# Performance work log

Hardware: AMD Instinct MI355X
Metric: run time of the kernel (lower is better)

The kernel has to match this reference:

```python
import jax, jax.numpy as jnp
import numpy as np

B, S, T, L, D, H = 32, 64, 256, 8, 128, 128
SIGNAL_SD = 1.0 - 0.001   # default signal_sds init
NOISE_SD = 0.01           # GP diagonal jitter (noise_sds) for Cholesky stability


def setup_inputs() -> dict:
    key = jax.random.key(0)
    ks = jax.random.split(key, 8)
    X = jax.random.normal(ks[0], (B, T, D), dtype=jnp.float32)
    times = (jnp.arange(T, dtype=jnp.float32) / T) * 10.0  # span [0, 10)
    log_taus = jax.random.normal(ks[1], (L,), dtype=jnp.float32) * 0.1 + jnp.log(0.5)
    log_R_diag = jax.random.normal(ks[2], (D,), dtype=jnp.float32) * 0.1
    W1 = jax.random.normal(ks[3], (L, H), dtype=jnp.float32) / np.sqrt(L)
    b1 = jnp.zeros((H,), dtype=jnp.float32)
    W2 = jax.random.normal(ks[4], (H, D), dtype=jnp.float32) / np.sqrt(H)
    b2 = jnp.zeros((D,), dtype=jnp.float32)
    eps = jax.random.normal(ks[5], (B, S, L, T), dtype=jnp.float32)
    return {"X": X, "times": times, "log_taus": log_taus, "log_R_diag": log_R_diag,
            "W1": W1, "b1": b1, "W2": W2, "b2": b2, "eps": eps}


def reference(X, times, log_taus, log_R_diag, W1, b1, W2, b2, eps):
    taus = jnp.exp(log_taus)            # [L]
    r = jnp.exp(log_R_diag)             # [D] diagonal of R

    # --- GP prior kernel matrices (squared-exponential SDE kernel), one per latent dim ---
    dt = times[:, None] - times[None, :]                       # [T,T]
    K = (SIGNAL_SD ** 2) * jnp.exp(-(dt ** 2)[None] / (2.0 * (taus ** 2)[:, None, None]))
    K = K + (NOISE_SD ** 2) * jnp.eye(T, dtype=K.dtype)        # [L,T,T]
    Lc = jnp.linalg.cholesky(K)                                # [L,T,T]

    # --- reparameterized prior samples: z = Lc @ eps ---
    z = jnp.einsum('lut,bslt->bslu', Lc, eps)                  # [B,S,L,T]
    Z = jnp.transpose(z, (0, 1, 3, 2))                         # [B,S,T,L]

    # --- decoder MLP: latent -> manifold mean in observation space ---
    h = jnp.tanh(jnp.einsum('bstl,lh->bsth', Z, W1) + b1)      # [B,S,T,H]
    mu = jnp.einsum('bsth,hd->bstd', h, W2) + b2               # [B,S,T,D]

    # --- diagonal-R Gaussian log_prob per timestep, closed form ---
    diff = X[:, None, :, :] - mu                               # [B,S,T,D]
    quad = jnp.sum(diff * diff / r, axis=-1)                   # [B,S,T]
    log_norm = 0.5 * (jnp.sum(log_R_diag) + D * jnp.log(2.0 * jnp.pi))
    logp = -0.5 * quad - log_norm                              # [B,S,T]

    # --- sum over time, logsumexp over MC samples ---
    ll = jnp.sum(logp, axis=2)                                 # [B,S]
    nll = -(jax.scipy.special.logsumexp(ll, axis=1) - jnp.log(jnp.float32(S)))
    return nll                                                 # [B]
```

## Files before the change

### kernel.cpp

```cpp
#include <hip/hip_runtime.h>
#include <hip/hip_bf16.h>
#include <math.h>

#define B_ 32
#define S_ 64
#define T_ 256
#define L_ 8
#define D_ 128
#define H_ 128

typedef __attribute__((ext_vector_type(8))) short short8;
typedef __attribute__((ext_vector_type(4))) short short4v;
typedef __attribute__((ext_vector_type(4))) float float4v;
typedef __attribute__((ext_vector_type(4))) int int4v;

__device__ __forceinline__ short f2bf(float x) {
  __hip_bfloat16 h = __float2bfloat16(x);
  return *reinterpret_cast<short*>(&h);
}

__device__ __forceinline__ float rdlane(float x, int sl) {
  return __int_as_float(__builtin_amdgcn_readlane(__float_as_int(x), sl));
}
__device__ __forceinline__ float dpp_shr1(float x, float tailv) {
  int r = __builtin_amdgcn_update_dpp(__float_as_int(tailv), __float_as_int(x),
                                      0x138, 0xF, 0xF, false);
  return __int_as_float(r);
}

__global__ __launch_bounds__(64) void k_chol_prep(
    const float* __restrict__ times, const float* __restrict__ log_taus,
    __hip_bfloat16* __restrict__ Lcbf_,
    const float* __restrict__ W1, const float* __restrict__ W2,
    __hip_bfloat16* __restrict__ W1T, __hip_bfloat16* __restrict__ W2T)
{
  __shared__ short panel[256][68];
  const int bi = blockIdx.x;
  const int j = threadIdx.x;

  if (bi >= 8) {
    const int base = (bi - 8) * 64 + j;
    for (int idx = base; idx < H_ * D_; idx += 4096) {
      const int cc = idx >> 7, h = idx & 127;
      const int n = cc & 15, nt = cc >> 4;
      const int d = n * 8 + nt;
      W2T[(size_t)cc * H_ + h] = __float2bfloat16(W2[(size_t)h * D_ + d]);
    }
    for (int idx = base; idx < L_ * H_; idx += 4096) {
      const int li = idx >> 7, h = idx & 127;
      const int msrc = 32 * (h >> 5) + 2 * (h & 15) + ((h >> 4) & 1);
      W1T[(size_t)h * L_ + li] = __float2bfloat16(W1[(size_t)li * H_ + msrc]);
    }
    return;
  }

  const int l = bi;
  short* Lbf = (short*)Lcbf_ + (size_t)l * T_ * T_;

  const float tau = expf(log_taus[l]);
  const float inv2tau2 = 0.5f / (tau * tau);
  const float sig2 = 0.999f * 0.999f;
  const float t0 = times[0];

  const float c0 = sig2 + 1e-4f;
  const float isc0 = 1.0f / sqrtf(c0);

  float u[4], v[4];
#pragma unroll
  for (int c = 0; c < 4; ++c) {
    const int d = c * 64 + j;
    const float dt = times[d] - t0;
    float cv = sig2 * __expf(-dt * dt * inv2tau2);
    if (d == 0) cv = c0;
    u[c] = cv * isc0;
    v[c] = (d == 0) ? 0.0f : u[c];
  }

#pragma unroll
  for (int p = 0; p < 4; ++p) {
    for (int kk = 0; kk < 64; ++kk) {
      const float uk = rdlane(u[p], kk);
      const float vk = rdlane(v[p], kk);
      const float dd = fmaxf(__builtin_fmaf(uk, uk, -vk * vk), 1e-20f);
      const float rr = __builtin_amdgcn_rsqf(dd);
      const float s = uk * rr;
      const float sr = vk * rr;

      float up[4];
#pragma unroll
      for (int c = 0; c < 4; ++c) {
        if (c >= p) {
          const float uc = u[c], vc = v[c];
          up[c] = s * uc - sr * vc;
          v[c]  = s * vc - sr * uc;
          const float val = (c > p || j >= kk) ? up[c] : 0.0f;
          panel[(c - p) * 64 + j][kk] = f2bf(val);
        }
      }
#pragma unroll
      for (int c = 3; c >= 0; --c) {
        if (c >= p) {
          const float tail = (c > p) ? rdlane(up[c - 1], 63) : 0.0f;
          u[c] = dpp_shr1(up[c], tail);
        }
      }
    }
    __syncthreads();
    const int rpt = 256 - 64 * p;
    const int rsub = j >> 4, cp = (j & 15) * 4;
    for (int i0 = 0; i0 < rpt; i0 += 4) {
      const int pr = i0 + rsub;
      short4v vv = *(const short4v*)&panel[pr][cp];
      *(short4v*)&Lbf[((size_t)(p * 64 + pr) << 8) + p * 64 + cp] = vv;
    }
    __syncthreads();
  }
}

__global__ __launch_bounds__(256) void k_zgemm(
    const float* __restrict__ eps, const __hip_bfloat16* __restrict__ Lcbf_,
    __hip_bfloat16* __restrict__ Zg)
{
  __shared__ __align__(16) short E[32][264];
  const int bi = blockIdx.x;
  const int l = bi & 7, bs0 = (bi >> 3) * 32;
  const int tid = threadIdx.x, w = tid >> 6, lane = tid & 63;
  const int n = lane & 15, q = lane >> 4;
  const short* Lb = (const short*)Lcbf_ + (size_t)l * T_ * T_;

  {
    const int row = tid >> 3, part = tid & 7;
    const float* src = eps + ((size_t)(bs0 + row) * L_ + l) * T_;
#pragma unroll
    for (int g = 0; g < 8; ++g) {
      const int c = (part + g * 8) * 4;
      float4v f = *(const float4v*)(src + c);
      short4v o;
#pragma unroll
      for (int jj = 0; jj < 4; ++jj) o[jj] = f2bf(f[jj]);
      *(short4v*)&E[row][c] = o;
    }
  }
  __syncthreads();

  float4v acc[4][2];
#pragma unroll
  for (int mi = 0; mi < 4; ++mi)
#pragma unroll
    for (int nt = 0; nt < 2; ++nt) acc[mi][nt] = (float4v){0.f, 0.f, 0.f, 0.f};

  const int kmax = ((15 - w + 2) >> 1) << 5;
  for (int k0 = 0; k0 < kmax; k0 += 32) {
    short8 bfrg[2];
#pragma unroll
    for (int nt = 0; nt < 2; ++nt)
      bfrg[nt] = *(const short8*)&E[nt * 16 + n][k0 + q * 8];
#pragma unroll
    for (int mi = 0; mi < 4; ++mi) {
      const int tile = (mi == 0) ? w : (mi == 1) ? (15 - w) : (mi == 2) ? (7 - w) : (8 + w);
      const int kc = ((tile + 2) >> 1) << 5;
      if (k0 < kc) {
        const int u = tile * 16 + n;
        const short8 afr = *(const short8*)&Lb[((size_t)u << 8) + k0 + q * 8];
#pragma unroll
        for (int nt = 0; nt < 2; ++nt)
          acc[mi][nt] = __builtin_amdgcn_mfma_f32_16x16x32_bf16(afr, bfrg[nt], acc[mi][nt], 0, 0, 0);
      }
    }
  }
  __syncthreads();

#pragma unroll
  for (int mi = 0; mi < 4; ++mi) {
    const int tile = (mi == 0) ? w : (mi == 1) ? (15 - w) : (mi == 2) ? (7 - w) : (8 + w);
#pragma unroll
    for (int nt = 0; nt < 2; ++nt) {
      short4v o;
#pragma unroll
      for (int r = 0; r < 4; ++r) o[r] = f2bf(acc[mi][nt][r]);
      *(short4v*)&E[nt * 16 + n][tile * 16 + q * 4] = o;
    }
  }
  __syncthreads();

  {
    const int row = tid >> 3, part = tid & 7;
    short* dst = (short*)Zg + ((size_t)l * (B_ * S_) + bs0 + row) * T_;
#pragma unroll
    for (int g = 0; g < 4; ++g) {
      const int c = (g * 8 + part) * 8;
      *(short8*)&dst[c] = *(const short8*)&E[row][c];
    }
  }
}

__global__ __launch_bounds__(256, 4) void k_decode(
    const float* __restrict__ X, const __hip_bfloat16* __restrict__ Zg,
    const __hip_bfloat16* __restrict__ W1T, const float* __restrict__ b1,
    const __hip_bfloat16* __restrict__ W2T, const float* __restrict__ b2,
    const float* __restrict__ log_R, float* __restrict__ ll)
{
  __shared__ __align__(16) short Zt[256][8];
  __shared__ __align__(16) __hip_bfloat16 hS[32][136];
  __shared__ float redbuf[4];

  const int bid = blockIdx.x;
  const int bs = (bid & 7) * 256 + (bid >> 3);
  const int b = bs >> 6;
  const int tid = threadIdx.x;
  const int w = tid >> 6, lane = tid & 63;
  const int n = lane & 15, q = lane >> 4;
  const unsigned short* Zs = (const unsigned short*)Zg;
  const short* W1s = (const short*)W1T;
  const short* W2s = (const short*)W2T;

  {
    const size_t base = (size_t)bs * T_ + tid;
    const size_t lstr = (size_t)(B_ * S_) * T_;
    unsigned int p0 = (unsigned int)Zs[base]            | ((unsigned int)Zs[base + lstr]     << 16);
    unsigned int p1 = (unsigned int)Zs[base + 2 * lstr] | ((unsigned int)Zs[base + 3 * lstr] << 16);
    unsigned int p2 = (unsigned int)Zs[base + 4 * lstr] | ((unsigned int)Zs[base + 5 * lstr] << 16);
    unsigned int p3 = (unsigned int)Zs[base + 6 * lstr] | ((unsigned int)Zs[base + 7 * lstr] << 16);
    int4v zi = {(int)p0, (int)p1, (int)p2, (int)p3};
    *(int4v*)&Zt[tid][0] = zi;
  }

  float sLR = log_R[lane] + log_R[lane + 64];
#pragma unroll
  for (int off = 32; off >= 1; off >>= 1) sLR += __shfl_xor(sLR, off);

  const float L22 = 2.8853900817779268f;
  const int d0 = n * 8 + 2 * w;
  const int hc = 32 * w + 2 * n;
  float invr2[2], b22[2], pb[2];
#pragma unroll
  for (int jj = 0; jj < 2; ++jj) {
    invr2[jj] = expf(-log_R[d0 + jj]);
    b22[jj] = b2[d0 + jj];
    pb[jj] = b1[hc + jj] * L22;
  }

  const short8 zero8 = {0, 0, 0, 0, 0, 0, 0, 0};
  short8 w1f[2];
  short8 bfr[2][4];
#pragma unroll
  for (int jj = 0; jj < 2; ++jj) {
    const int c = (2 * w + jj) * 16 + n;
    short8 v = zero8;
    if (q == 0) v = *(const short8*)&W1s[(size_t)c * L_];
    w1f[jj] = v;
#pragma unroll
    for (int ks = 0; ks < 4; ++ks)
      bfr[jj][ks] = *(const short8*)&W2s[(size_t)c * H_ + ks * 32 + q * 8];
  }

  float qsum = 0.0f;
  __syncthreads();

#pragma unroll 1
  for (int ph = 0; ph < 8; ++ph) {
    short* hp = (short*)hS + (q * 4) * 136 + hc;
#pragma unroll 1
    for (int mi = 0; mi < 2; ++mi) {
      short8 zf = zero8;
      if (q == 0) zf = *(const short8*)&Zt[ph * 32 + mi * 16 + n][0];
      float4v c0 = __builtin_amdgcn_mfma_f32_16x16x32_bf16(zf, w1f[0], (float4v){0.f,0.f,0.f,0.f}, 0, 0, 0);
      float4v c1 = __builtin_amdgcn_mfma_f32_16x16x32_bf16(zf, w1f[1], (float4v){0.f,0.f,0.f,0.f}, 0, 0, 0);
#pragma unroll
      for (int r = 0; r < 4; ++r) {
        const float a0 = __builtin_fmaf(c0[r], L22, pb[0]);
        const float a1 = __builtin_fmaf(c1[r], L22, pb[1]);
        const float p0 = __builtin_amdgcn_exp2f(a0) + 1.f;
        const float p1 = __builtin_amdgcn_exp2f(a1) + 1.f;
        const float rj = __builtin_amdgcn_rcpf(p0 * p1);
        const float h0 = __builtin_fmaf(-2.f * p1, rj, 1.f);
        const float h1 = __builtin_fmaf(-2.f * p0, rj, 1.f);
        float2 hv2; hv2.x = h0; hv2.y = h1;
        *reinterpret_cast<__hip_bfloat162*>(hp + r * 136) = __float22bfloat162_rn(hv2);
      }
      hp += 16 * 136;
    }
    __syncthreads();
#pragma unroll 1
    for (int mi = 0; mi < 2; ++mi) {
      short8 af[4];
#pragma unroll
      for (int ks = 0; ks < 4; ++ks)
        af[ks] = *(const short8*)&hS[mi * 16 + n][ks * 32 + q * 8];
      float4v acc0 = (float4v){0.f, 0.f, 0.f, 0.f};
      float4v acc1 = (float4v){0.f, 0.f, 0.f, 0.f};
#pragma unroll
      for (int ks = 0; ks < 4; ++ks) {
        acc0 = __builtin_amdgcn_mfma_f32_16x16x32_bf16(af[ks], bfr[0][ks], acc0, 0, 0, 0);
        acc1 = __builtin_amdgcn_mfma_f32_16x16x32_bf16(af[ks], bfr[1][ks], acc1, 0, 0, 0);
      }
      const int tbase = ph * 32 + mi * 16 + q * 4;
#pragma unroll
      for (int r = 0; r < 4; ++r) {
        const int t = tbase + r;
        const float2 xv = *(const float2*)(X + (((size_t)b << 8) + t) * D_ + d0);
        float diff0 = xv.x - (acc0[r] + b22[0]);
        float diff1 = xv.y - (acc1[r] + b22[1]);
        qsum += diff0 * diff0 * invr2[0] + diff1 * diff1 * invr2[1];
      }
    }
    __syncthreads();
  }

#pragma unroll
  for (int off = 32; off >= 1; off >>= 1) qsum += __shfl_xor(qsum, off);
  if (lane == 0) redbuf[w] = qsum;
  __syncthreads();
  if (tid == 0) {
    float Q = redbuf[0] + redbuf[1] + redbuf[2] + redbuf[3];
    float log_norm = 0.5f * (sLR + (float)D_ * 1.8378770664093453f);
    ll[bs] = -0.5f * Q - (float)T_ * log_norm;
  }
}

__global__ __launch_bounds__(64) void k_lse(
    const float* __restrict__ ll, float* __restrict__ out)
{
  const int b = blockIdx.x;
  const int s = threadIdx.x;
  float v = ll[b * 64 + s];
  float m = v;
#pragma unroll
  for (int off = 32; off >= 1; off >>= 1) m = fmaxf(m, __shfl_xor(m, off));
  float e = __expf(v - m);
#pragma unroll
  for (int off = 32; off >= 1; off >>= 1) e += __shfl_xor(e, off);
  if (s == 0) out[b] = -(m + __logf(e) - 4.1588830833596715f);
}

extern "C" void kernel_launch(void* const* d_in, const int* in_sizes, int n_in,
                              void* d_out, int out_size, void* d_ws, size_t ws_size,
                              hipStream_t stream) {
  const float* X        = (const float*)d_in[0];
  const float* times    = (const float*)d_in[1];
  const float* log_taus = (const float*)d_in[2];
  const float* log_R    = (const float*)d_in[3];
  const float* W1       = (const float*)d_in[4];
  const float* b1       = (const float*)d_in[5];
  const float* W2       = (const float*)d_in[6];
  const float* b2       = (const float*)d_in[7];
  const float* eps      = (const float*)d_in[8];
  float* out = (float*)d_out;

  char* ws = (char*)d_ws;
  __hip_bfloat16* Lcbf = (__hip_bfloat16*)(ws);
  __hip_bfloat16* Zg   = (__hip_bfloat16*)(ws + 1048576);
  float* ll            = (float*)(ws + 9437184);
  __hip_bfloat16* W2T  = (__hip_bfloat16*)(ws + 9445376);
  __hip_bfloat16* W1T  = (__hip_bfloat16*)(ws + 9478144);

  hipLaunchKernelGGL(k_chol_prep, dim3(72),   dim3(64),  0, stream,
                     times, log_taus, Lcbf, W1, W2, W1T, W2T);
  hipLaunchKernelGGL(k_zgemm,     dim3(512),  dim3(256), 0, stream, eps, Lcbf, Zg);
  hipLaunchKernelGGL(k_decode,    dim3(2048), dim3(256), 0, stream, X, Zg, W1T, b1, W2T, b2, log_R, ll);
  hipLaunchKernelGGL(k_lse,       dim3(32),   dim3(64),  0, stream, ll, out);
}
```

Baseline: 153.9 us.

## Double-buffer hidden activations in decode kernel and raise occupancy hint

Splits the hidden-activation LDS buffer into two halves so the tanh layer for the next phase is computed while the second GEMM of the current phase reads the other half. This cuts one block barrier per phase and lets the first-layer MFMA and transcendental work overlap with the second-layer MFMA and X loads. The launch bound now asks for 8 blocks per CU instead of 4, which pushes the compiler to use fewer registers and may cause spills. The LDS footprint per block also grows.

```diff
diff --git a/kernel.cpp b/kernel.cpp
--- a/kernel.cpp
+++ b/kernel.cpp
@@ -194,14 +194,14 @@
   }
 }
 
-__global__ __launch_bounds__(256, 4) void k_decode(
+__global__ __launch_bounds__(256, 8) void k_decode(
     const float* __restrict__ X, const __hip_bfloat16* __restrict__ Zg,
     const __hip_bfloat16* __restrict__ W1T, const float* __restrict__ b1,
     const __hip_bfloat16* __restrict__ W2T, const float* __restrict__ b2,
     const float* __restrict__ log_R, float* __restrict__ ll)
 {
   __shared__ __align__(16) short Zt[256][8];
-  __shared__ __align__(16) __hip_bfloat16 hS[32][136];
+  __shared__ __align__(16) __hip_bfloat16 hS[2][32][136];
   __shared__ float redbuf[4];
 
   const int bid = blockIdx.x;
@@ -257,36 +257,43 @@
   float qsum = 0.0f;
   __syncthreads();
 
+#define PRODUCE(pp)                                                           \
+  {                                                                           \
+    short* hp = (short*)hS + ((pp) & 1) * (32 * 136) + (q * 4) * 136 + hc;    \
+    _Pragma("unroll")                                                         \
+    for (int mi = 0; mi < 2; ++mi) {                                          \
+      short8 zf = zero8;                                                      \
+      if (q == 0) zf = *(const short8*)&Zt[(pp) * 32 + mi * 16 + n][0];       \
+      float4v c0 = __builtin_amdgcn_mfma_f32_16x16x32_bf16(zf, w1f[0], (float4v){0.f,0.f,0.f,0.f}, 0, 0, 0); \
+      float4v c1 = __builtin_amdgcn_mfma_f32_16x16x32_bf16(zf, w1f[1], (float4v){0.f,0.f,0.f,0.f}, 0, 0, 0); \
+      _Pragma("unroll")                                                       \
+      for (int r = 0; r < 4; ++r) {                                           \
+        const float a0 = __builtin_fmaf(c0[r], L22, pb[0]);                   \
+        const float a1 = __builtin_fmaf(c1[r], L22, pb[1]);                   \
+        const float p0 = __builtin_amdgcn_exp2f(a0) + 1.f;                    \
+        const float p1 = __builtin_amdgcn_exp2f(a1) + 1.f;                    \
+        const float rj = __builtin_amdgcn_rcpf(p0 * p1);                      \
+        const float h0 = __builtin_fmaf(-2.f * p1, rj, 1.f);                  \
+        const float h1 = __builtin_fmaf(-2.f * p0, rj, 1.f);                  \
+        float2 hv2; hv2.x = h0; hv2.y = h1;                                   \
+        *reinterpret_cast<__hip_bfloat162*>(hp + r * 136) = __float22bfloat162_rn(hv2); \
+      }                                                                       \
+      hp += 16 * 136;                                                         \
+    }                                                                         \
+  }
+
+  PRODUCE(0)
+  __syncthreads();
+
 #pragma unroll 1
   for (int ph = 0; ph < 8; ++ph) {
-    short* hp = (short*)hS + (q * 4) * 136 + hc;
-#pragma unroll 1
-    for (int mi = 0; mi < 2; ++mi) {
-      short8 zf = zero8;
-      if (q == 0) zf = *(const short8*)&Zt[ph * 32 + mi * 16 + n][0];
-      float4v c0 = __builtin_amdgcn_mfma_f32_16x16x32_bf16(zf, w1f[0], (float4v){0.f,0.f,0.f,0.f}, 0, 0, 0);
-      float4v c1 = __builtin_amdgcn_mfma_f32_16x16x32_bf16(zf, w1f[1], (float4v){0.f,0.f,0.f,0.f}, 0, 0, 0);
-#pragma unroll
-      for (int r = 0; r < 4; ++r) {
-        const float a0 = __builtin_fmaf(c0[r], L22, pb[0]);
-        const float a1 = __builtin_fmaf(c1[r], L22, pb[1]);
-        const float p0 = __builtin_amdgcn_exp2f(a0) + 1.f;
-        const float p1 = __builtin_amdgcn_exp2f(a1) + 1.f;
-        const float rj = __builtin_amdgcn_rcpf(p0 * p1);
-        const float h0 = __builtin_fmaf(-2.f * p1, rj, 1.f);
-        const float h1 = __builtin_fmaf(-2.f * p0, rj, 1.f);
-        float2 hv2; hv2.x = h0; hv2.y = h1;
-        *reinterpret_cast<__hip_bfloat162*>(hp + r * 136) = __float22bfloat162_rn(hv2);
-      }
-      hp += 16 * 136;
-    }
-    __syncthreads();
+    const int pb_idx = ph & 1;
 #pragma unroll 1
     for (int mi = 0; mi < 2; ++mi) {
       short8 af[4];
 #pragma unroll
       for (int ks = 0; ks < 4; ++ks)
-        af[ks] = *(const short8*)&hS[mi * 16 + n][ks * 32 + q * 8];
+        af[ks] = *(const short8*)&hS[pb_idx][mi * 16 + n][ks * 32 + q * 8];
       float4v acc0 = (float4v){0.f, 0.f, 0.f, 0.f};
       float4v acc1 = (float4v){0.f, 0.f, 0.f, 0.f};
 #pragma unroll
@@ -304,8 +311,10 @@
         qsum += diff0 * diff0 * invr2[0] + diff1 * diff1 * invr2[1];
       }
     }
+    if (ph < 7) PRODUCE(ph + 1)
     __syncthreads();
   }
+#undef PRODUCE
 
 #pragma unroll
   for (int off = 32; off >= 1; off >>= 1) qsum += __shfl_xor(qsum, off);
```

Result: no change. 156.6 us (+1.8%).

## Precast eps to bf16 in idle Cholesky-kernel blocks, read directly in zgemm

Applied to the files above, without the earlier changes.

Extra blocks are added to the Cholesky/prep kernel that convert eps from fp32 to bf16 into a workspace buffer laid out per latent dim. This overlaps the conversion with the serial Cholesky work. The zgemm kernel then reads B fragments straight from global bf16 memory instead of staging them through LDS, which removes a sync and the in-kernel conversion. The cost is an extra 8 MB write and read round trip through global memory, and the B fragments are now uncoalesced global loads repeated across waves. It only takes effect when the workspace is large enough.

```diff
diff --git a/kernel.cpp b/kernel.cpp
--- a/kernel.cpp
+++ b/kernel.cpp
@@ -32,11 +32,35 @@
     const float* __restrict__ times, const float* __restrict__ log_taus,
     __hip_bfloat16* __restrict__ Lcbf_,
     const float* __restrict__ W1, const float* __restrict__ W2,
-    __hip_bfloat16* __restrict__ W1T, __hip_bfloat16* __restrict__ W2T)
+    __hip_bfloat16* __restrict__ W1T, __hip_bfloat16* __restrict__ W2T,
+    const float* __restrict__ eps, __hip_bfloat16* __restrict__ Eg)
 {
   __shared__ short panel[256][68];
   const int bi = blockIdx.x;
   const int j = threadIdx.x;
+
+  if (bi >= 72) {
+    short* EgS = (short*)Eg;
+    const int e = bi - 72;
+    const int sub = j >> 3, part = j & 7;
+#pragma unroll 1
+    for (int p = 0; p < 16; ++p) {
+      const int ri = e * 128 + p * 8 + sub;
+      const int l = ri & 7, bs = ri >> 3;
+      const float* src = eps + (size_t)ri * 256;
+      short* dst = EgS + ((size_t)(l << 11) + bs) * 256;
+#pragma unroll
+      for (int g = 0; g < 8; ++g) {
+        const int c = (part + g * 8) * 4;
+        float4v f = *(const float4v*)(src + c);
+        short4v o;
+#pragma unroll
+        for (int jj = 0; jj < 4; ++jj) o[jj] = f2bf(f[jj]);
+        *(short4v*)&dst[c] = o;
+      }
+    }
+    return;
+  }
 
   if (bi >= 8) {
     const int base = (bi - 8) * 64 + j;
@@ -118,8 +142,9 @@
 }
 
 __global__ __launch_bounds__(256) void k_zgemm(
-    const float* __restrict__ eps, const __hip_bfloat16* __restrict__ Lcbf_,
-    __hip_bfloat16* __restrict__ Zg)
+    const float* __restrict__ eps, const __hip_bfloat16* __restrict__ Eg,
+    const __hip_bfloat16* __restrict__ Lcbf_,
+    __hip_bfloat16* __restrict__ Zg, const int useEg)
 {
   __shared__ __align__(16) short E[32][264];
   const int bi = blockIdx.x;
@@ -128,7 +153,7 @@
   const int n = lane & 15, q = lane >> 4;
   const short* Lb = (const short*)Lcbf_ + (size_t)l * T_ * T_;
 
-  {
+  if (!useEg) {
     const int row = tid >> 3, part = tid & 7;
     const float* src = eps + ((size_t)(bs0 + row) * L_ + l) * T_;
 #pragma unroll
@@ -140,8 +165,8 @@
       for (int jj = 0; jj < 4; ++jj) o[jj] = f2bf(f[jj]);
       *(short4v*)&E[row][c] = o;
     }
-  }
-  __syncthreads();
+    __syncthreads();
+  }
 
   float4v acc[4][2];
 #pragma unroll
@@ -150,21 +175,43 @@
     for (int nt = 0; nt < 2; ++nt) acc[mi][nt] = (float4v){0.f, 0.f, 0.f, 0.f};
 
   const int kmax = ((15 - w + 2) >> 1) << 5;
-  for (int k0 = 0; k0 < kmax; k0 += 32) {
-    short8 bfrg[2];
-#pragma unroll
-    for (int nt = 0; nt < 2; ++nt)
-      bfrg[nt] = *(const short8*)&E[nt * 16 + n][k0 + q * 8];
-#pragma unroll
-    for (int mi = 0; mi < 4; ++mi) {
-      const int tile = (mi == 0) ? w : (mi == 1) ? (15 - w) : (mi == 2) ? (7 - w) : (8 + w);
-      const int kc = ((tile + 2) >> 1) << 5;
-      if (k0 < kc) {
-        const int u = tile * 16 + n;
-        const short8 afr = *(const short8*)&Lb[((size_t)u << 8) + k0 + q * 8];
-#pragma unroll
-        for (int nt = 0; nt < 2; ++nt)
-          acc[mi][nt] = __builtin_amdgcn_mfma_f32_16x16x32_bf16(afr, bfrg[nt], acc[mi][nt], 0, 0, 0);
+  if (useEg) {
+    const short* Eb = (const short*)Eg + ((size_t)(l << 11) + bs0) * 256;
+    for (int k0 = 0; k0 < kmax; k0 += 32) {
+      short8 bfrg[2];
+#pragma unroll
+      for (int nt = 0; nt < 2; ++nt)
+        bfrg[nt] = *(const short8*)&Eb[(size_t)(nt * 16 + n) * 256 + k0 + q * 8];
+#pragma unroll
+      for (int mi = 0; mi < 4; ++mi) {
+        const int tile = (mi == 0) ? w : (mi == 1) ? (15 - w) : (mi == 2) ? (7 - w) : (8 + w);
+        const int kc = ((tile + 2) >> 1) << 5;
+        if (k0 < kc) {
+          const int u = tile * 16 + n;
+          const short8 afr = *(const short8*)&Lb[((size_t)u << 8) + k0 + q * 8];
+#pragma unroll
+          for (int nt = 0; nt < 2; ++nt)
+            acc[mi][nt] = __builtin_amdgcn_mfma_f32_16x16x32_bf16(afr, bfrg[nt], acc[mi][nt], 0, 0, 0);
+        }
+      }
+    }
+  } else {
+    for (int k0 = 0; k0 < kmax; k0 += 32) {
+      short8 bfrg[2];
+#pragma unroll
+      for (int nt = 0; nt < 2; ++nt)
+        bfrg[nt] = *(const short8*)&E[nt * 16 + n][k0 + q * 8];
+#pragma unroll
+      for (int mi = 0; mi < 4; ++mi) {
+        const int tile = (mi == 0) ? w : (mi == 1) ? (15 - w) : (mi == 2) ? (7 - w) : (8 + w);
+        const int kc = ((tile + 2) >> 1) << 5;
+        if (k0 < kc) {
+          const int u = tile * 16 + n;
+          const short8 afr = *(const short8*)&Lb[((size_t)u << 8) + k0 + q * 8];
+#pragma unroll
+          for (int nt = 0; nt < 2; ++nt)
+            acc[mi][nt] = __builtin_amdgcn_mfma_f32_16x16x32_bf16(afr, bfrg[nt], acc[mi][nt], 0, 0, 0);
+        }
       }
     }
   }
@@ -353,10 +400,13 @@
   float* ll            = (float*)(ws + 9437184);
   __hip_bfloat16* W2T  = (__hip_bfloat16*)(ws + 9445376);
   __hip_bfloat16* W1T  = (__hip_bfloat16*)(ws + 9478144);
-
-  hipLaunchKernelGGL(k_chol_prep, dim3(72),   dim3(64),  0, stream,
-                     times, log_taus, Lcbf, W1, W2, W1T, W2T);
-  hipLaunchKernelGGL(k_zgemm,     dim3(512),  dim3(256), 0, stream, eps, Lcbf, Zg);
+  __hip_bfloat16* Eg   = (__hip_bfloat16*)(ws + 9480192);
+
+  const int useEg = (ws_size >= (size_t)9480192 + 8388608) ? 1 : 0;
+
+  hipLaunchKernelGGL(k_chol_prep, dim3(useEg ? 200 : 72), dim3(64), 0, stream,
+                     times, log_taus, Lcbf, W1, W2, W1T, W2T, eps, Eg);
+  hipLaunchKernelGGL(k_zgemm,     dim3(512),  dim3(256), 0, stream, eps, Eg, Lcbf, Zg, useEg);
   hipLaunchKernelGGL(k_decode,    dim3(2048), dim3(256), 0, stream, X, Zg, W1T, b1, W2T, b2, log_R, ll);
   hipLaunchKernelGGL(k_lse,       dim3(32),   dim3(64),  0, stream, ll, out);
 }
```

Measured after the change: 155.1 us. About the same (+0.8%).
